# Optimization experiments

Hardware: AMD Instinct MI355X
Metric: run time of the kernel (lower is better)

The kernel has to match this reference:

```python
import jax, jax.numpy as jnp
import numpy as np

EMBED = 1024
HEADS = 16
HEAD_DIM = EMBED // HEADS
N, S = 2, 2048


def setup_inputs() -> dict:
    key0 = jax.random.key(0)
    ks = jax.random.split(key0, 9)
    inp = {
        "value": jax.random.normal(ks[0], (N, S, EMBED), dtype=jnp.float32),
        "key": jax.random.normal(ks[1], (N, S, EMBED), dtype=jnp.float32),
        "query": jax.random.normal(ks[2], (N, S, EMBED), dtype=jnp.float32),
        "mask": jax.random.randint(ks[3], (N, 1, S, S), 0, 2, dtype=jnp.int32),
        # per-head projection weights (nn.Linear: y = x @ W.T), bias=False
        "Wv": jax.random.normal(ks[4], (HEAD_DIM, HEAD_DIM), dtype=jnp.float32) / np.sqrt(HEAD_DIM),
        "Wk": jax.random.normal(ks[5], (HEAD_DIM, HEAD_DIM), dtype=jnp.float32) / np.sqrt(HEAD_DIM),
        "Wq": jax.random.normal(ks[6], (HEAD_DIM, HEAD_DIM), dtype=jnp.float32) / np.sqrt(HEAD_DIM),
        "Wo": jax.random.normal(ks[7], (EMBED, EMBED), dtype=jnp.float32) / np.sqrt(EMBED),
        "bo": jax.random.normal(ks[8], (EMBED,), dtype=jnp.float32) * 0.01,
    }
    return inp


def reference(value, key, query, mask, Wv, Wk, Wq, Wo, bo):
    n, q_len = query.shape[0], query.shape[1]
    v = value.reshape(n, -1, HEADS, HEAD_DIM)
    k = key.reshape(n, -1, HEADS, HEAD_DIM)
    q = query.reshape(n, -1, HEADS, HEAD_DIM)
    # per-head linear projections (x @ W.T)
    v = jnp.einsum('nlhd,ed->nlhe', v, Wv)
    k = jnp.einsum('nlhd,ed->nlhe', k, Wk)
    q = jnp.einsum('nlhd,ed->nlhe', q, Wq)
    energy = jnp.einsum('nqhd,nkhd->nhqk', q, k)
    # faithful to the source: masked_fill with +1e20 where mask == 0
    energy = jnp.where(mask == 0, jnp.float32(1e20), energy)
    attention = jax.nn.softmax(energy / jnp.sqrt(jnp.float32(EMBED)), axis=3)
    out = jnp.einsum('nhql,nlhd->nqhd', attention, v)
    out = out.reshape(n, q_len, EMBED)
    return out @ Wo.T + bo
```

## Files before the change

### kernel.cpp

```cpp
#include <hip/hip_runtime.h>
#include <hip/hip_bf16.h>
#include <stdint.h>

#define SEQ 2048

typedef __attribute__((ext_vector_type(8))) short s8v;
typedef __attribute__((ext_vector_type(4))) float f4v;

static __device__ __forceinline__ unsigned short f2bf(float f) {
  union { float f; unsigned u; } x; x.f = f;
  return (unsigned short)((x.u + 0x7FFFu + ((x.u >> 16) & 1u)) >> 16);
}

static __device__ __forceinline__ void glds16(const unsigned short* g, unsigned short* l) {
  auto* lp = reinterpret_cast<__attribute__((address_space(3))) unsigned int*>(
      reinterpret_cast<uintptr_t>(l));
  const auto* gp = reinterpret_cast<const __attribute__((address_space(1))) unsigned int*>(
      reinterpret_cast<uintptr_t>(g));
  __builtin_amdgcn_global_load_lds(gp, lp, 16, 0, 0);
}

__global__ void k_prep(const float* __restrict__ V, const float* __restrict__ Wv,
                       const float* __restrict__ Wo, const int* __restrict__ mask,
                       unsigned short* __restrict__ Vb, unsigned short* __restrict__ W2t,
                       unsigned short* __restrict__ Mb, float* __restrict__ rcnt) {
  const int bid = blockIdx.x, tid = threadIdx.x;
  __shared__ float wv_s[64 * 64];
  if (bid < 2048) {
    int t = bid * 256 + tid;
    const float4* src = (const float4*)V;
    float4 a = src[t * 2], b = src[t * 2 + 1];
    ushort4 p0, p1;
    p0.x = f2bf(a.x); p0.y = f2bf(a.y); p0.z = f2bf(a.z); p0.w = f2bf(a.w);
    p1.x = f2bf(b.x); p1.y = f2bf(b.y); p1.z = f2bf(b.z); p1.w = f2bf(b.w);
    ((ushort4*)Vb)[t * 2] = p0; ((ushort4*)Vb)[t * 2 + 1] = p1;
  } else if (bid < 6144) {
    int b = bid - 2048;
#pragma unroll
    for (int i = 0; i < 4; ++i) { int c = tid + i * 256; ((float4*)wv_s)[c] = ((const float4*)Wv)[c]; }
    __syncthreads();
    const int f = b >> 2;
    const int g = ((b & 3) << 8) + tid;
    const int h = g >> 6, dd = g & 63;
    const float* wo = Wo + f * 1024 + h * 64;
    float acc = 0.f;
#pragma unroll
    for (int e = 0; e < 64; ++e) acc += wv_s[e * 64 + dd] * wo[e];
    W2t[(size_t)f * 1024 + g] = f2bf(acc);
  } else {
    int row = bid - 6144;
    const int4* mrow = (const int4*)(mask + (size_t)row * SEQ);
    int4 a = mrow[tid * 2], b = mrow[tid * 2 + 1];
    const unsigned short ONE = 0x3F80;
    ushort4 o0, o1;
    o0.x = (a.x == 0) ? ONE : 0; o0.y = (a.y == 0) ? ONE : 0;
    o0.z = (a.z == 0) ? ONE : 0; o0.w = (a.w == 0) ? ONE : 0;
    o1.x = (b.x == 0) ? ONE : 0; o1.y = (b.y == 0) ? ONE : 0;
    o1.z = (b.z == 0) ? ONE : 0; o1.w = (b.w == 0) ? ONE : 0;
    ushort4* orow = (ushort4*)(Mb + (size_t)row * SEQ);
    orow[tid * 2] = o0; orow[tid * 2 + 1] = o1;
    int* red = (int*)wv_s;
    red[tid] = (a.x == 0) + (a.y == 0) + (a.z == 0) + (a.w == 0)
             + (b.x == 0) + (b.y == 0) + (b.z == 0) + (b.w == 0);
    __syncthreads();
    for (int s = 128; s > 0; s >>= 1) { if (tid < s) red[tid] += red[tid + s]; __syncthreads(); }
    if (tid == 0) rcnt[row] = 1.0f / (float)red[0];
  }
}

template <int MODE>
__global__ __launch_bounds__(256, 2) void k_gemm(
    const unsigned short* __restrict__ A,
    const unsigned short* __restrict__ Bt,
    int Kdim, void* __restrict__ OutP,
    const float* __restrict__ rcnt, const float* __restrict__ bo) {
  __shared__ __align__(16) unsigned short As[2][64 * 64];
  __shared__ __align__(16) unsigned short Bs[2][128 * 64];

  size_t outbase = 0;
  if (MODE == 1) {
    const int z = blockIdx.z;
    A    += (size_t)z * SEQ * SEQ;
    Bt   += (size_t)z * 1024 * SEQ;
    rcnt += (size_t)z * SEQ;
    outbase = (size_t)z * SEQ * 1024;
  }

  const int tid = threadIdx.x;
  const int wave = tid >> 6, lane = tid & 63;
  const int quad = lane >> 4, l15 = lane & 15;
  const int wm = (wave & 1) * 32, wn = (wave >> 1) * 64;
  const int bm0 = blockIdx.y * 64, bn0 = blockIdx.x * 128;

  const int ra = tid >> 3, pa = tid & 7;
  const unsigned short* ga0 = A + (size_t)(bm0 + ra) * Kdim + (pa ^ ((ra >> 1) & 7)) * 8;
  const unsigned short* ga1 = A + (size_t)(bm0 + 32 + ra) * Kdim + (pa ^ (((ra + 32) >> 1) & 7)) * 8;
  const unsigned short* gb[4];
#pragma unroll
  for (int j = 0; j < 4; ++j) {
    int rb = (tid + j * 256) >> 3;
    gb[j] = Bt + (size_t)(bn0 + rb) * Kdim + ((pa ^ ((rb >> 1) & 7))) * 8;
  }

  f4v acc[2][4];
#pragma unroll
  for (int i = 0; i < 2; ++i)
#pragma unroll
    for (int j = 0; j < 4; ++j) acc[i][j] = (f4v){0.f, 0.f, 0.f, 0.f};

  auto stage = [&](int buf, int k) {
    glds16(ga0 + k, As[buf] + tid * 8);
    glds16(ga1 + k, As[buf] + (tid + 256) * 8);
#pragma unroll
    for (int j = 0; j < 4; ++j) glds16(gb[j] + k, Bs[buf] + (tid + j * 256) * 8);
  };
  auto compute = [&](int buf) {
#pragma unroll
    for (int kg = 0; kg < 2; ++kg) {
      const int pos = ((kg * 4 + quad) ^ ((l15 >> 1) & 7)) * 8;
      s8v af[2], bf[4];
#pragma unroll
      for (int t = 0; t < 2; ++t)
        af[t] = *(const s8v*)(As[buf] + (wm + t * 16 + l15) * 64 + pos);
#pragma unroll
      for (int u = 0; u < 4; ++u)
        bf[u] = *(const s8v*)(Bs[buf] + (wn + u * 16 + l15) * 64 + pos);
#pragma unroll
      for (int tm = 0; tm < 2; ++tm)
#pragma unroll
        for (int tn = 0; tn < 4; ++tn)
          acc[tm][tn] = __builtin_amdgcn_mfma_f32_16x16x32_bf16(af[tm], bf[tn], acc[tm][tn], 0, 0, 0);
    }
  };

  stage(0, 0);
  for (int k0 = 0; k0 < Kdim; k0 += 128) {
    __syncthreads();
    if (k0 + 64 < Kdim) stage(1, k0 + 64);
    compute(0);
    __syncthreads();
    if (k0 + 128 < Kdim) stage(0, k0 + 128);
    compute(1);
  }

#pragma unroll
  for (int tm = 0; tm < 2; ++tm)
#pragma unroll
    for (int tn = 0; tn < 4; ++tn) {
      int gm0 = bm0 + wm + tm * 16 + quad * 4;
      int f   = bn0 + wn + tn * 16 + l15;
      if (MODE == 0) {
        int batch = gm0 >> 11, l0 = gm0 & 2047;
        ushort4 pk;
        pk.x = f2bf(acc[tm][tn][0]); pk.y = f2bf(acc[tm][tn][1]);
        pk.z = f2bf(acc[tm][tn][2]); pk.w = f2bf(acc[tm][tn][3]);
        *(ushort4*)((unsigned short*)OutP + (size_t)batch * (1024 * SEQ) + (size_t)f * SEQ + l0) = pk;
      } else {
        float bof = bo[f];
        float* out = (float*)OutP + outbase;
#pragma unroll
        for (int r = 0; r < 4; ++r) {
          int row = gm0 + r;
          out[(size_t)row * 1024 + f] = acc[tm][tn][r] * rcnt[row] + bof;
        }
      }
    }
}

extern "C" void kernel_launch(void* const* d_in, const int* in_sizes, int n_in,
                              void* d_out, int out_size, void* d_ws, size_t ws_size,
                              hipStream_t stream) {
  const float* V   = (const float*)d_in[0];
  const int* mask  = (const int*)d_in[3];
  const float* Wv  = (const float*)d_in[4];
  const float* Wo  = (const float*)d_in[7];
  const float* bo  = (const float*)d_in[8];

  char* ws = (char*)d_ws;
  unsigned short* W2t  = (unsigned short*)ws;
  unsigned short* Ut   = (unsigned short*)(ws + ((size_t)2  << 20));
  unsigned short* Vb   = (unsigned short*)(ws + ((size_t)10 << 20));
  unsigned short* Mb   = (unsigned short*)(ws + ((size_t)18 << 20));
  float*          rcnt = (float*)(ws + ((size_t)34 << 20));

  k_prep<<<10240, 256, 0, stream>>>(V, Wv, Wo, mask, Vb, W2t, Mb, rcnt);
  k_gemm<0><<<dim3(8, 64), 256, 0, stream>>>(Vb, W2t, 1024, Ut, nullptr, nullptr);
  k_gemm<1><<<dim3(8, 32, 2), 256, 0, stream>>>(Mb, Ut, SEQ, d_out, rcnt, bo);
}
```

Baseline: 170.3 us.

## Use 128x128 tiles with split-K and atomic accumulation in output GEMM

Replaces the templated GEMM with two specialised kernels. The mask-by-value GEMM now uses 128x128 tiles and splits K into two halves, accumulating into the output with float atomicAdd after the prep kernel zeroes it. The aim is more data reuse per tile while keeping enough blocks. It adds a zeroing pass and atomic traffic on the whole output, and makes the floating-point summation order nondeterministic.

Result: slower. 189.0 us (+11.0%).

```diff
diff --git a/kernel.cpp b/kernel.cpp
--- a/kernel.cpp
+++ b/kernel.cpp
@@ -23,7 +23,8 @@
 __global__ void k_prep(const float* __restrict__ V, const float* __restrict__ Wv,
                        const float* __restrict__ Wo, const int* __restrict__ mask,
                        unsigned short* __restrict__ Vb, unsigned short* __restrict__ W2t,
-                       unsigned short* __restrict__ Mb, float* __restrict__ rcnt) {
+                       unsigned short* __restrict__ Mb, float* __restrict__ rcnt,
+                       float* __restrict__ OutZ) {
   const int bid = blockIdx.x, tid = threadIdx.x;
   __shared__ float wv_s[64 * 64];
   if (bid < 2048) {
@@ -47,7 +48,7 @@
 #pragma unroll
     for (int e = 0; e < 64; ++e) acc += wv_s[e * 64 + dd] * wo[e];
     W2t[(size_t)f * 1024 + g] = f2bf(acc);
-  } else {
+  } else if (bid < 10240) {
     int row = bid - 6144;
     const int4* mrow = (const int4*)(mask + (size_t)row * SEQ);
     int4 a = mrow[tid * 2], b = mrow[tid * 2 + 1];
@@ -65,27 +66,19 @@
     __syncthreads();
     for (int s = 128; s > 0; s >>= 1) { if (tid < s) red[tid] += red[tid + s]; __syncthreads(); }
     if (tid == 0) rcnt[row] = 1.0f / (float)red[0];
-  }
-}
-
-template <int MODE>
-__global__ __launch_bounds__(256, 2) void k_gemm(
-    const unsigned short* __restrict__ A,
-    const unsigned short* __restrict__ Bt,
-    int Kdim, void* __restrict__ OutP,
-    const float* __restrict__ rcnt, const float* __restrict__ bo) {
+  } else {
+    int t = (bid - 10240) * 256 + tid;
+    float4 z = {0.f, 0.f, 0.f, 0.f};
+    ((float4*)OutZ)[t * 2] = z; ((float4*)OutZ)[t * 2 + 1] = z;
+  }
+}
+
+__global__ __launch_bounds__(256, 2) void k_gemm0(
+    const unsigned short* __restrict__ A, const unsigned short* __restrict__ Bt,
+    unsigned short* __restrict__ Ut) {
   __shared__ __align__(16) unsigned short As[2][64 * 64];
   __shared__ __align__(16) unsigned short Bs[2][128 * 64];
-
-  size_t outbase = 0;
-  if (MODE == 1) {
-    const int z = blockIdx.z;
-    A    += (size_t)z * SEQ * SEQ;
-    Bt   += (size_t)z * 1024 * SEQ;
-    rcnt += (size_t)z * SEQ;
-    outbase = (size_t)z * SEQ * 1024;
-  }
-
+  const int Kdim = 1024;
   const int tid = threadIdx.x;
   const int wave = tid >> 6, lane = tid & 63;
   const int quad = lane >> 4, l15 = lane & 15;
@@ -149,20 +142,95 @@
     for (int tn = 0; tn < 4; ++tn) {
       int gm0 = bm0 + wm + tm * 16 + quad * 4;
       int f   = bn0 + wn + tn * 16 + l15;
-      if (MODE == 0) {
-        int batch = gm0 >> 11, l0 = gm0 & 2047;
-        ushort4 pk;
-        pk.x = f2bf(acc[tm][tn][0]); pk.y = f2bf(acc[tm][tn][1]);
-        pk.z = f2bf(acc[tm][tn][2]); pk.w = f2bf(acc[tm][tn][3]);
-        *(ushort4*)((unsigned short*)OutP + (size_t)batch * (1024 * SEQ) + (size_t)f * SEQ + l0) = pk;
-      } else {
-        float bof = bo[f];
-        float* out = (float*)OutP + outbase;
-#pragma unroll
-        for (int r = 0; r < 4; ++r) {
-          int row = gm0 + r;
-          out[(size_t)row * 1024 + f] = acc[tm][tn][r] * rcnt[row] + bof;
-        }
+      int batch = gm0 >> 11, l0 = gm0 & 2047;
+      ushort4 pk;
+      pk.x = f2bf(acc[tm][tn][0]); pk.y = f2bf(acc[tm][tn][1]);
+      pk.z = f2bf(acc[tm][tn][2]); pk.w = f2bf(acc[tm][tn][3]);
+      *(ushort4*)(Ut + (size_t)batch * (1024 * SEQ) + (size_t)f * SEQ + l0) = pk;
+    }
+}
+
+__global__ __launch_bounds__(256, 2) void k_gemm1(
+    const unsigned short* __restrict__ A,
+    const unsigned short* __restrict__ Bt,
+    float* __restrict__ Out,
+    const float* __restrict__ rcnt, const float* __restrict__ bo) {
+  __shared__ __align__(16) unsigned short As[2][128 * 64];
+  __shared__ __align__(16) unsigned short Bs[2][128 * 64];
+  const int z = blockIdx.z, batch = z & 1, ks = z >> 1;
+  A    += (size_t)batch * SEQ * SEQ + ks * 1024;
+  Bt   += (size_t)batch * 1024 * SEQ + ks * 1024;
+  rcnt += (size_t)batch * SEQ;
+  Out  += (size_t)batch * SEQ * 1024;
+
+  const int tid = threadIdx.x;
+  const int wave = tid >> 6, lane = tid & 63;
+  const int quad = lane >> 4, l15 = lane & 15;
+  const int wm = (wave >> 1) * 64, wn = (wave & 1) * 64;
+  const int bm0 = blockIdx.y * 128, bn0 = blockIdx.x * 128;
+
+  const unsigned short* ga[4];
+  const unsigned short* gb[4];
+#pragma unroll
+  for (int j = 0; j < 4; ++j) {
+    int c = tid + j * 256, r = c >> 3, p = c & 7;
+    ga[j] = A  + (size_t)(bm0 + r) * SEQ + (p ^ ((r >> 1) & 7)) * 8;
+    gb[j] = Bt + (size_t)(bn0 + r) * SEQ + (p ^ ((r >> 1) & 7)) * 8;
+  }
+
+  f4v acc[4][4];
+#pragma unroll
+  for (int i = 0; i < 4; ++i)
+#pragma unroll
+    for (int j = 0; j < 4; ++j) acc[i][j] = (f4v){0.f, 0.f, 0.f, 0.f};
+
+  auto stage = [&](int buf, int k) {
+#pragma unroll
+    for (int j = 0; j < 4; ++j) {
+      glds16(ga[j] + k, As[buf] + (tid + j * 256) * 8);
+      glds16(gb[j] + k, Bs[buf] + (tid + j * 256) * 8);
+    }
+  };
+  auto compute = [&](int buf) {
+#pragma unroll
+    for (int kg = 0; kg < 2; ++kg) {
+      const int pos = ((kg * 4 + quad) ^ ((l15 >> 1) & 7)) * 8;
+      s8v af[4], bf[4];
+#pragma unroll
+      for (int t = 0; t < 4; ++t)
+        af[t] = *(const s8v*)(As[buf] + (wm + t * 16 + l15) * 64 + pos);
+#pragma unroll
+      for (int u = 0; u < 4; ++u)
+        bf[u] = *(const s8v*)(Bs[buf] + (wn + u * 16 + l15) * 64 + pos);
+#pragma unroll
+      for (int tm = 0; tm < 4; ++tm)
+#pragma unroll
+        for (int tn = 0; tn < 4; ++tn)
+          acc[tm][tn] = __builtin_amdgcn_mfma_f32_16x16x32_bf16(af[tm], bf[tn], acc[tm][tn], 0, 0, 0);
+    }
+  };
+
+  stage(0, 0);
+  for (int k0 = 0; k0 < 1024; k0 += 128) {
+    __syncthreads();
+    if (k0 + 64 < 1024) stage(1, k0 + 64);
+    compute(0);
+    __syncthreads();
+    if (k0 + 128 < 1024) stage(0, k0 + 128);
+    compute(1);
+  }
+
+#pragma unroll
+  for (int tm = 0; tm < 4; ++tm)
+#pragma unroll
+    for (int tn = 0; tn < 4; ++tn) {
+      int gm0 = bm0 + wm + tm * 16 + quad * 4;
+      int f   = bn0 + wn + tn * 16 + l15;
+      float bof = (ks == 0) ? bo[f] : 0.f;
+#pragma unroll
+      for (int r = 0; r < 4; ++r) {
+        int row = gm0 + r;
+        atomicAdd(Out + (size_t)row * 1024 + f, acc[tm][tn][r] * rcnt[row] + bof);
       }
     }
 }
@@ -183,7 +251,7 @@
   unsigned short* Mb   = (unsigned short*)(ws + ((size_t)18 << 20));
   float*          rcnt = (float*)(ws + ((size_t)34 << 20));
 
-  k_prep<<<10240, 256, 0, stream>>>(V, Wv, Wo, mask, Vb, W2t, Mb, rcnt);
-  k_gemm<0><<<dim3(8, 64), 256, 0, stream>>>(Vb, W2t, 1024, Ut, nullptr, nullptr);
-  k_gemm<1><<<dim3(8, 32, 2), 256, 0, stream>>>(Mb, Ut, SEQ, d_out, rcnt, bo);
-}
+  k_prep<<<12288, 256, 0, stream>>>(V, Wv, Wo, mask, Vb, W2t, Mb, rcnt, (float*)d_out);
+  k_gemm0<<<dim3(8, 64), 256, 0, stream>>>(Vb, W2t, Ut);
+  k_gemm1<<<dim3(8, 16, 4), 256, 0, stream>>>(Mb, Ut, (float*)d_out, rcnt, bo);
+}
```
